# Kernel optimization log

Hardware: AMD Instinct MI355X
Metric: run time of the kernel (lower is better)

The kernel has to match this reference:

```python
import jax, jax.numpy as jnp
import numpy as np

H, W, C = 1024, 1024, 17  # texture height, width, channels (16 features + 1 homogeneous)
N = 2_000_000             # number of UV query points


def setup_inputs() -> dict:
    key = jax.random.key(0)
    k1, k2 = jax.random.split(key)
    texture = jax.random.uniform(k1, (H, W, C), dtype=jnp.float32)
    uv_tensor = jax.random.uniform(k2, (N, 2), dtype=jnp.float32)  # uv in [0,1)
    return {"texture": texture, "uv_tensor": uv_tensor}


def _slice_texture(texture, uv):
    """Bilinear texture lookup at continuous UV coords (SliceTexture.apply).

    texture: [H, W, C], uv: [N, 2] in [0,1] -> [N, C]
    """
    h, w, _ = texture.shape
    x = uv[:, 0] * (w - 1)
    y = uv[:, 1] * (h - 1)
    x0 = jnp.clip(jnp.floor(x), 0, w - 2).astype(jnp.int32)
    y0 = jnp.clip(jnp.floor(y), 0, h - 2).astype(jnp.int32)
    fx = (x - x0)[:, None]
    fy = (y - y0)[:, None]
    # four corner gathers (irregular access)
    t00 = texture[y0, x0]
    t01 = texture[y0, x0 + 1]
    t10 = texture[y0 + 1, x0]
    t11 = texture[y0 + 1, x0 + 1]
    top = t00 * (1.0 - fx) + t01 * fx
    bot = t10 * (1.0 - fx) + t11 * fx
    return top * (1.0 - fy) + bot * fy  # [N, C]


def reference(texture, uv_tensor):
    values_not_normalized = _slice_texture(texture, uv_tensor)  # [N, C]
    val_dim = values_not_normalized.shape[1] - 1
    homogeneous = values_not_normalized[:, val_dim:val_dim + 1]  # [N, 1]
    values = values_not_normalized[:, :val_dim] / (homogeneous + 1e-5)  # [N, C-1]
    return values, homogeneous, values_not_normalized
```

## Files before the change

### kernel.cpp

```cpp
#include <hip/hip_runtime.h>

#define TEX_H 1024
#define TEX_W 1024
#define TEX_C 17

__global__ __launch_bounds__(256) void slice_texture_kernel(
    const float* __restrict__ tex,
    const float* __restrict__ uv,
    float* __restrict__ out,
    int n)
{
    int i = blockIdx.x * blockDim.x + threadIdx.x;
    if (i >= n) return;

    float2 p = ((const float2*)uv)[i];

    float x = p.x * (float)(TEX_W - 1);
    float y = p.y * (float)(TEX_H - 1);
    float x0f = fminf(fmaxf(floorf(x), 0.0f), (float)(TEX_W - 2));
    float y0f = fminf(fmaxf(floorf(y), 0.0f), (float)(TEX_H - 2));
    int x0 = (int)x0f;
    int y0 = (int)y0f;
    float fx = x - x0f;
    float fy = y - y0f;
    float gx = 1.0f - fx;
    float gy = 1.0f - fy;

    const float* r0 = tex + ((size_t)y0 * TEX_W + (size_t)x0) * TEX_C;
    const float* r1 = r0 + (size_t)TEX_W * TEX_C;

    float vnn[TEX_C];
#pragma unroll
    for (int c = 0; c < TEX_C; ++c) {
        float t00 = r0[c];
        float t01 = r0[c + TEX_C];
        float t10 = r1[c];
        float t11 = r1[c + TEX_C];
        float top = t00 * gx + t01 * fx;
        float bot = t10 * gx + t11 * fx;
        vnn[c] = top * gy + bot * fy;
    }

    float h = vnn[16];
    float inv = 1.0f / (h + 1e-5f);

    float4* vrow = (float4*)(out + (size_t)i * 16);
#pragma unroll
    for (int q = 0; q < 4; ++q) {
        float4 v;
        v.x = vnn[q * 4 + 0] * inv;
        v.y = vnn[q * 4 + 1] * inv;
        v.z = vnn[q * 4 + 2] * inv;
        v.w = vnn[q * 4 + 3] * inv;
        vrow[q] = v;
    }

    out[(size_t)n * 16 + i] = h;

    float* vout = out + (size_t)n * 17 + (size_t)i * 17;
#pragma unroll
    for (int c = 0; c < TEX_C; ++c) {
        vout[c] = vnn[c];
    }
}

extern "C" void kernel_launch(void* const* d_in, const int* in_sizes, int n_in,
                              void* d_out, int out_size, void* d_ws, size_t ws_size,
                              hipStream_t stream) {
    const float* tex = (const float*)d_in[0];
    const float* uv  = (const float*)d_in[1];
    float* out = (float*)d_out;
    int n = in_sizes[1] / 2;

    const int block = 256;
    const int grid = (n + block - 1) / block;
    slice_texture_kernel<<<grid, block, 0, stream>>>(tex, uv, out, n);
}
```

Before: 465.3 us.

## Bin UV queries by 8x8 texture tile before bilinear gather

Adds a counting-sort pipeline (zero, histogram, scan, scatter) that groups query points by 8x8 texture tile. A process kernel then gathers texels in tile order, so neighbouring threads hit nearby texture rows and get better cache reuse. In exchange it adds five launches, atomics, a 32 MB record array round-trip, and scattered output writes, with a fallback direct kernel when the workspace is too small.

```diff
diff --git a/kernel.cpp b/kernel.cpp
--- a/kernel.cpp
+++ b/kernel.cpp
@@ -3,30 +3,95 @@
 #define TEX_H 1024
 #define TEX_W 1024
 #define TEX_C 17
+#define TILE_SHIFT 3
+#define TILES_X (TEX_W >> TILE_SHIFT)
+#define TILES_Y (TEX_H >> TILE_SHIFT)
+#define NTILES (TILES_X * TILES_Y)
 
-__global__ __launch_bounds__(256) void slice_texture_kernel(
-    const float* __restrict__ tex,
-    const float* __restrict__ uv,
-    float* __restrict__ out,
-    int n)
-{
-    int i = blockIdx.x * blockDim.x + threadIdx.x;
-    if (i >= n) return;
-
-    float2 p = ((const float2*)uv)[i];
-
+__device__ __forceinline__ void decode_uv(float2 p, int& x0, int& y0,
+                                          float& fx, float& fy) {
     float x = p.x * (float)(TEX_W - 1);
     float y = p.y * (float)(TEX_H - 1);
     float x0f = fminf(fmaxf(floorf(x), 0.0f), (float)(TEX_W - 2));
     float y0f = fminf(fmaxf(floorf(y), 0.0f), (float)(TEX_H - 2));
-    int x0 = (int)x0f;
-    int y0 = (int)y0f;
-    float fx = x - x0f;
-    float fy = y - y0f;
+    x0 = (int)x0f;
+    y0 = (int)y0f;
+    fx = x - x0f;
+    fy = y - y0f;
+}
+
+__global__ __launch_bounds__(256) void k_zero(unsigned int* __restrict__ cursor) {
+    int i = blockIdx.x * blockDim.x + threadIdx.x;
+    if (i < NTILES) cursor[i] = 0u;
+}
+
+__global__ __launch_bounds__(256) void k_hist(const float* __restrict__ uv,
+                                              unsigned int* __restrict__ cursor,
+                                              int n) {
+    int i = blockIdx.x * blockDim.x + threadIdx.x;
+    if (i >= n) return;
+    float2 p = ((const float2*)uv)[i];
+    int x0, y0; float fx, fy;
+    decode_uv(p, x0, y0, fx, fy);
+    int tile = (y0 >> TILE_SHIFT) * TILES_X + (x0 >> TILE_SHIFT);
+    atomicAdd(&cursor[tile], 1u);
+}
+
+__global__ __launch_bounds__(256) void k_scan(unsigned int* __restrict__ cursor) {
+    __shared__ unsigned int part[256];
+    __shared__ unsigned int excl[256];
+    int t = threadIdx.x;
+    const int per = NTILES / 256;
+    unsigned int sum = 0;
+    for (int k = 0; k < per; ++k) sum += cursor[t * per + k];
+    part[t] = sum;
+    __syncthreads();
+    if (t == 0) {
+        unsigned int run = 0;
+        for (int j = 0; j < 256; ++j) { excl[j] = run; run += part[j]; }
+    }
+    __syncthreads();
+    unsigned int run = excl[t];
+    for (int k = 0; k < per; ++k) {
+        unsigned int c = cursor[t * per + k];
+        cursor[t * per + k] = run;
+        run += c;
+    }
+}
+
+__global__ __launch_bounds__(256) void k_scatter(const float* __restrict__ uv,
+                                                 unsigned int* __restrict__ cursor,
+                                                 uint4* __restrict__ records,
+                                                 int n) {
+    int i = blockIdx.x * blockDim.x + threadIdx.x;
+    if (i >= n) return;
+    float2 p = ((const float2*)uv)[i];
+    int x0, y0; float fx, fy;
+    decode_uv(p, x0, y0, fx, fy);
+    int tile = (y0 >> TILE_SHIFT) * TILES_X + (x0 >> TILE_SHIFT);
+    unsigned int pos = atomicAdd(&cursor[tile], 1u);
+    uint4 rec;
+    rec.x = (unsigned int)i;
+    rec.y = (unsigned int)(y0 * TEX_W + x0);
+    rec.z = __float_as_uint(fx);
+    rec.w = __float_as_uint(fy);
+    records[pos] = rec;
+}
+
+__global__ __launch_bounds__(256) void k_process(const float* __restrict__ tex,
+                                                 const uint4* __restrict__ records,
+                                                 float* __restrict__ out,
+                                                 int n) {
+    int g = blockIdx.x * blockDim.x + threadIdx.x;
+    if (g >= n) return;
+    uint4 rec = records[g];
+    unsigned int idx = rec.x;
+    float fx = __uint_as_float(rec.z);
+    float fy = __uint_as_float(rec.w);
     float gx = 1.0f - fx;
     float gy = 1.0f - fy;
 
-    const float* r0 = tex + ((size_t)y0 * TEX_W + (size_t)x0) * TEX_C;
+    const float* r0 = tex + (size_t)rec.y * TEX_C;
     const float* r1 = r0 + (size_t)TEX_W * TEX_C;
 
     float vnn[TEX_C];
@@ -44,6 +109,48 @@
     float h = vnn[16];
     float inv = 1.0f / (h + 1e-5f);
 
+    float4* vrow = (float4*)(out + (size_t)idx * 16);
+#pragma unroll
+    for (int q = 0; q < 4; ++q) {
+        float4 v;
+        v.x = vnn[q * 4 + 0] * inv;
+        v.y = vnn[q * 4 + 1] * inv;
+        v.z = vnn[q * 4 + 2] * inv;
+        v.w = vnn[q * 4 + 3] * inv;
+        vrow[q] = v;
+    }
+
+    out[(size_t)n * 16 + idx] = h;
+
+    float* vout = out + (size_t)n * 17 + (size_t)idx * 17;
+#pragma unroll
+    for (int c = 0; c < TEX_C; ++c) vout[c] = vnn[c];
+}
+
+__global__ __launch_bounds__(256) void k_direct(const float* __restrict__ tex,
+                                                const float* __restrict__ uv,
+                                                float* __restrict__ out,
+                                                int n) {
+    int i = blockIdx.x * blockDim.x + threadIdx.x;
+    if (i >= n) return;
+    float2 p = ((const float2*)uv)[i];
+    int x0, y0; float fx, fy;
+    decode_uv(p, x0, y0, fx, fy);
+    float gx = 1.0f - fx;
+    float gy = 1.0f - fy;
+    const float* r0 = tex + ((size_t)y0 * TEX_W + (size_t)x0) * TEX_C;
+    const float* r1 = r0 + (size_t)TEX_W * TEX_C;
+    float vnn[TEX_C];
+#pragma unroll
+    for (int c = 0; c < TEX_C; ++c) {
+        float t00 = r0[c];
+        float t01 = r0[c + TEX_C];
+        float t10 = r1[c];
+        float t11 = r1[c + TEX_C];
+        vnn[c] = (t00 * gx + t01 * fx) * gy + (t10 * gx + t11 * fx) * fy;
+    }
+    float h = vnn[16];
+    float inv = 1.0f / (h + 1e-5f);
     float4* vrow = (float4*)(out + (size_t)i * 16);
 #pragma unroll
     for (int q = 0; q < 4; ++q) {
@@ -54,14 +161,10 @@
         v.w = vnn[q * 4 + 3] * inv;
         vrow[q] = v;
     }
-
     out[(size_t)n * 16 + i] = h;
-
     float* vout = out + (size_t)n * 17 + (size_t)i * 17;
 #pragma unroll
-    for (int c = 0; c < TEX_C; ++c) {
-        vout[c] = vnn[c];
-    }
+    for (int c = 0; c < TEX_C; ++c) vout[c] = vnn[c];
 }
 
 extern "C" void kernel_launch(void* const* d_in, const int* in_sizes, int n_in,
@@ -73,6 +176,20 @@
     int n = in_sizes[1] / 2;
 
     const int block = 256;
-    const int grid = (n + block - 1) / block;
-    slice_texture_kernel<<<grid, block, 0, stream>>>(tex, uv, out, n);
+    const int gridN = (n + block - 1) / block;
+
+    size_t need = (size_t)NTILES * 4 + (size_t)n * 16;
+    if (ws_size < need) {
+        k_direct<<<gridN, block, 0, stream>>>(tex, uv, out, n);
+        return;
+    }
+
+    unsigned int* cursor = (unsigned int*)d_ws;
+    uint4* records = (uint4*)((char*)d_ws + (size_t)NTILES * 4);
+
+    k_zero<<<(NTILES + block - 1) / block, block, 0, stream>>>(cursor);
+    k_hist<<<gridN, block, 0, stream>>>(uv, cursor, n);
+    k_scan<<<1, block, 0, stream>>>(cursor);
+    k_scatter<<<gridN, block, 0, stream>>>(uv, cursor, records, n);
+    k_process<<<gridN, block, 0, stream>>>(tex, records, out, n);
 }
```

Result: slower. 691.0 us (+48.5%).
